# Kernel tuning notes

Measured on AMD Instinct MI355X. Metric: run time of the kernel, lower is better.

The kernel has to match this reference:

```python
import jax, jax.numpy as jnp
import numpy as np


def setup_inputs() -> dict:
    key = jax.random.key(0)
    k1, k2 = jax.random.split(key)
    B, T, D, K = 8, 4096, 256, 1024
    z = jax.random.normal(k1, (B, T, D), dtype=jnp.float32)
    codebook = jax.random.uniform(k2, (K, D), dtype=jnp.float32)
    return {"z": z, "codebook": codebook}


def reference(z, codebook):
    # Squared L2 distance via dot-product decomposition (same argmin as
    # the broadcasted squared-difference in the original module, without
    # materializing the (B,T,K,D) intermediate).
    #   ||z - c||^2 = ||z||^2 - 2 z.c + ||c||^2
    z_sq = jnp.sum(z * z, axis=-1, keepdims=True)            # (B,T,1)
    c_sq = jnp.sum(codebook * codebook, axis=-1)             # (K,)
    cross = jnp.einsum("btd,kd->btk", z, codebook)           # (B,T,K)
    l2_distance = z_sq - 2.0 * cross + c_sq                  # (B,T,K)
    codebook_indices = jnp.argmin(l2_distance, axis=-1)      # (B,T)
    z_q = codebook[codebook_indices]                         # (B,T,D)
    # Straight-through estimator
    z_q = z + jax.lax.stop_gradient(z_q - z)
    return (z_q, codebook_indices)
```

## Files before the change

### kernel.cpp

```cpp
#include <hip/hip_runtime.h>
#include <math.h>

#define NTOK   32768
#define NDIM   256
#define NCODE  1024
#define CHUNK  4096

typedef _Float16 f16x8 __attribute__((ext_vector_type(8)));
typedef float    f32x4 __attribute__((ext_vector_type(4)));

__device__ __forceinline__ void gld_lds16(const void* g, void* l) {
    __builtin_amdgcn_global_load_lds(
        (const __attribute__((address_space(1))) void*)g,
        (__attribute__((address_space(3))) void*)l, 16, 0, 0);
}

__global__ __launch_bounds__(256) void prep_cb(
        const float* __restrict__ cb,
        _Float16* __restrict__ ch, _Float16* __restrict__ cl,
        float* __restrict__ csq) {
    const int L   = blockIdx.x * 256 + threadIdx.x;
    const int row = L >> 5;
    const int g   = L & 31;

    const float* src = cb + (size_t)row * NDIM + g * 8;
    float4 a0 = *(const float4*)src;
    float4 a1 = *(const float4*)(src + 4);
    float v[8] = {a0.x, a0.y, a0.z, a0.w, a1.x, a1.y, a1.z, a1.w};
    f16x8 hi, lo;
    float s = 0.f;
    #pragma unroll
    for (int e = 0; e < 8; ++e) {
        _Float16 h = (_Float16)v[e];
        hi[e] = h;
        lo[e] = (_Float16)(v[e] - (float)h);
        s += v[e] * v[e];
    }
    const int r = row & 127;
    const size_t dst = (size_t)((row >> 7) * 8 + (g >> 2)) * CHUNK
                     + (r >> 4) * 512 + (g & 3) * 128 + (r & 15) * 8;
    *(f16x8*)&ch[dst] = hi;
    *(f16x8*)&cl[dst] = lo;
    #pragma unroll
    for (int off = 16; off > 0; off >>= 1) s += __shfl_down(s, off, 32);
    if ((threadIdx.x & 31) == 0) csq[row] = s;
}


#define STAGE(h, buf)                                                          \
    do {                                                                       \
        const size_t _sb = (size_t)(h) * 16384 + (size_t)tid * 8;              \
        _Pragma("unroll")                                                      \
        for (int _i = 0; _i < 4; ++_i) {                                       \
            gld_lds16(ch + _sb + _i * 4096, &Bs[buf][0][w * 512 + _i * 4096]); \
            gld_lds16(cl + _sb + _i * 4096, &Bs[buf][1][w * 512 + _i * 4096]); \
        }                                                                      \
    } while (0)

#define COMPUTE(kh, buf)                                                       \
    do {                                                                       \
        _Pragma("unroll")                                                      \
        for (int _k4 = 0; _k4 < 4; ++_k4) {                                    \
            f16x8 fbh[4], fbl[4];                                              \
            _Pragma("unroll")                                                  \
            for (int _t = 0; _t < 4; ++_t) {                                   \
                const int _off = _k4 * 4096 + (nx * 4 + _t) * 512              \
                               + quad * 128 + lr * 8;                          \
                fbh[_t] = *(const f16x8*)&Bs[buf][0][_off];                    \
                fbl[_t] = *(const f16x8*)&Bs[buf][1][_off];                    \
            }                                                                  \
            __builtin_amdgcn_s_setprio(1);                                     \
            _Pragma("unroll")                                                  \
            for (int _mt = 0; _mt < 2; ++_mt)                                  \
                _Pragma("unroll")                                              \
                for (int _t = 0; _t < 4; ++_t) {                               \
                    acc[_mt][_t] = __builtin_amdgcn_mfma_f32_16x16x32_f16(     \
                        ah[_mt][(kh) * 4 + _k4], fbh[_t], acc[_mt][_t], 0, 0, 0); \
                    acc[_mt][_t] = __builtin_amdgcn_mfma_f32_16x16x32_f16(     \
                        al[_mt][(kh) * 4 + _k4], fbh[_t], acc[_mt][_t], 0, 0, 0); \
                    acc[_mt][_t] = __builtin_amdgcn_mfma_f32_16x16x32_f16(     \
                        ah[_mt][(kh) * 4 + _k4], fbl[_t], acc[_mt][_t], 0, 0, 0); \
                }                                                              \
            __builtin_amdgcn_s_setprio(0);                                     \
        }                                                                      \
    } while (0)

__global__ __launch_bounds__(512, 2) void vq_main(
        const float* __restrict__ z,
        const _Float16* __restrict__ ch, const _Float16* __restrict__ cl,
        const float* __restrict__ csq, const float* __restrict__ cb,
        float* __restrict__ zq, float* __restrict__ io) {
    __shared__ _Float16 Bs[2][2][16384];

    const int tid  = threadIdx.x;
    const int w    = tid >> 6;
    const int lane = tid & 63;
    const int quad = lane >> 4, lr = lane & 15;
    const int my   = w >> 1, nx = w & 1;
    const int m0   = blockIdx.x * 128;

    STAGE(0, 0);

    f16x8 ah[2][8], al[2][8];
    #pragma unroll
    for (int mt = 0; mt < 2; ++mt) {
        const float* zp = z + (size_t)(m0 + my * 32 + mt * 16 + lr) * NDIM
                        + quad * 8;
        #pragma unroll
        for (int c = 0; c < 8; ++c) {
            float4 a0 = *(const float4*)(zp + c * 32);
            float4 a1 = *(const float4*)(zp + c * 32 + 4);
            float v[8] = {a0.x, a0.y, a0.z, a0.w, a1.x, a1.y, a1.z, a1.w};
            #pragma unroll
            for (int e = 0; e < 8; ++e) {
                _Float16 h = (_Float16)v[e];
                ah[mt][c][e] = h;
                al[mt][c][e] = (_Float16)(v[e] - (float)h);
            }
        }
    }

    float bv[2][4];
    int   bi[2][4];
    #pragma unroll
    for (int mt = 0; mt < 2; ++mt)
        #pragma unroll
        for (int r = 0; r < 4; ++r) { bv[mt][r] = INFINITY; bi[mt][r] = 0x7fffffff; }

    f32x4 acc[2][4];
    #pragma unroll
    for (int mt = 0; mt < 2; ++mt)
        #pragma unroll
        for (int t = 0; t < 4; ++t) acc[mt][t] = (f32x4){0.f, 0.f, 0.f, 0.f};

    for (int strip = 0; strip < 8; ++strip) {
        float cs[4];
        #pragma unroll
        for (int t = 0; t < 4; ++t)
            cs[t] = csq[strip * 128 + (nx * 4 + t) * 16 + lr];

        STAGE(2 * strip + 1, 1);
        asm volatile("s_waitcnt vmcnt(12)" ::: "memory");
        __builtin_amdgcn_s_barrier();
        __builtin_amdgcn_sched_barrier(0);
        COMPUTE(0, 0);
        __builtin_amdgcn_sched_barrier(0);
        __builtin_amdgcn_s_barrier();

        if (strip < 7) {
            STAGE(2 * strip + 2, 0);
            asm volatile("s_waitcnt vmcnt(8)" ::: "memory");
        } else {
            asm volatile("s_waitcnt vmcnt(0)" ::: "memory");
        }
        __builtin_amdgcn_s_barrier();
        __builtin_amdgcn_sched_barrier(0);
        COMPUTE(1, 1);
        __builtin_amdgcn_sched_barrier(0);
        __builtin_amdgcn_s_barrier();

        #pragma unroll
        for (int mt = 0; mt < 2; ++mt)
            #pragma unroll
            for (int r = 0; r < 4; ++r)
                #pragma unroll
                for (int t = 0; t < 4; ++t) {
                    float v = cs[t] - 2.0f * acc[mt][t][r];
                    int   n = strip * 128 + (nx * 4 + t) * 16 + lr;
                    if (v < bv[mt][r] || (v == bv[mt][r] && n < bi[mt][r])) {
                        bv[mt][r] = v; bi[mt][r] = n;
                    }
                }
        #pragma unroll
        for (int mt = 0; mt < 2; ++mt)
            #pragma unroll
            for (int t = 0; t < 4; ++t) acc[mt][t] = (f32x4){0.f, 0.f, 0.f, 0.f};
    }

    #pragma unroll
    for (int msk = 1; msk < 16; msk <<= 1)
        #pragma unroll
        for (int mt = 0; mt < 2; ++mt)
            #pragma unroll
            for (int r = 0; r < 4; ++r) {
                float ov = __shfl_xor(bv[mt][r], msk, 64);
                int   oi = __shfl_xor(bi[mt][r], msk, 64);
                if (ov < bv[mt][r] || (ov == bv[mt][r] && oi < bi[mt][r])) {
                    bv[mt][r] = ov; bi[mt][r] = oi;
                }
            }

    __syncthreads();
    float* sval  = (float*)&Bs[0][0][0];
    int*   sidx  = (int*)(sval + 256);
    int*   bestS = (int*)(sval + 512);

    if (lr == 0) {
        #pragma unroll
        for (int mt = 0; mt < 2; ++mt)
            #pragma unroll
            for (int r = 0; r < 4; ++r) {
                int row = my * 32 + mt * 16 + quad * 4 + r;
                sval[row * 2 + nx] = bv[mt][r];
                sidx[row * 2 + nx] = bi[mt][r];
            }
    }
    __syncthreads();

    if (tid < 128) {
        float v0 = sval[tid * 2], v1 = sval[tid * 2 + 1];
        int   i0 = sidx[tid * 2], i1 = sidx[tid * 2 + 1];
        bool take1 = (v1 < v0) || (v1 == v0 && i1 < i0);
        int best = take1 ? i1 : i0;
        bestS[tid] = best;
        io[m0 + tid] = (float)best;
    }
    __syncthreads();

    const int tr = tid >> 4, tc = tid & 15;
    #pragma unroll
    for (int p = 0; p < 4; ++p) {
        int row = p * 32 + tr;
        const float* src = cb + (size_t)bestS[row] * NDIM;
        float*       dst = zq + (size_t)(m0 + row) * NDIM;
        #pragma unroll
        for (int q = 0; q < 4; ++q) {
            int col = q * 64 + tc * 4;
            *(float4*)&dst[col] = *(const float4*)&src[col];
        }
    }
}

extern "C" void kernel_launch(void* const* d_in, const int* in_sizes, int n_in,
                              void* d_out, int out_size, void* d_ws, size_t ws_size,
                              hipStream_t stream) {
    const float* z  = (const float*)d_in[0];
    const float* cb = (const float*)d_in[1];

    float* zq = (float*)d_out;
    float* io = (float*)d_out + (size_t)NTOK * NDIM;

    _Float16* ch  = (_Float16*)d_ws;
    _Float16* cl  = ch + (size_t)NCODE * NDIM;
    float*    csq = (float*)(cl + (size_t)NCODE * NDIM);

    prep_cb<<<NCODE * 32 / 256, 256, 0, stream>>>(cb, ch, cl, csq);

    vq_main<<<NTOK / 128, 512, 0, stream>>>(z, ch, cl, csq, cb, zq, io);
}
```

Measured before the change: 151.6 us.

## Halve the token tile to 64 rows and split the codebook staging into quarter-strip stages

Each block now handles 64 tokens with 256 threads instead of 128 tokens with 512 threads. Codebook staging moves to quarter-strip (64-dim) double-buffered stages, which halves shared memory per block and gives four barrier-separated compute phases per strip. The sched_barrier fences are removed. The aim is more blocks per CU and a smaller LDS footprint to improve latency hiding, at the cost of twice as many blocks each re-reading the whole codebook, plus more barriers.

```diff
diff --git a/kernel.cpp b/kernel.cpp
--- a/kernel.cpp
+++ b/kernel.cpp
@@ -47,24 +47,26 @@
 }
 
 
-#define STAGE(h, buf)                                                          \
+#define STAGE(Q, buf)                                                          \
     do {                                                                       \
-        const size_t _sb = (size_t)(h) * 16384 + (size_t)tid * 8;              \
+        const size_t _sb = (size_t)(Q) * 8192 + w * 2048 + lane * 8;           \
+        const int    _lb = w * 2048;                                           \
         _Pragma("unroll")                                                      \
         for (int _i = 0; _i < 4; ++_i) {                                       \
-            gld_lds16(ch + _sb + _i * 4096, &Bs[buf][0][w * 512 + _i * 4096]); \
-            gld_lds16(cl + _sb + _i * 4096, &Bs[buf][1][w * 512 + _i * 4096]); \
+            gld_lds16(ch + _sb + _i * 512, &Bs[buf][0][_lb + _i * 512]);       \
+            gld_lds16(cl + _sb + _i * 512, &Bs[buf][1][_lb + _i * 512]);       \
         }                                                                      \
     } while (0)
 
-#define COMPUTE(kh, buf)                                                       \
+#define COMPUTE(q, buf)                                                        \
     do {                                                                       \
         _Pragma("unroll")                                                      \
-        for (int _k4 = 0; _k4 < 4; ++_k4) {                                    \
+        for (int _kc = 0; _kc < 2; ++_kc) {                                    \
+            const int _kg = (q) * 2 + _kc;                                     \
             f16x8 fbh[4], fbl[4];                                              \
             _Pragma("unroll")                                                  \
             for (int _t = 0; _t < 4; ++_t) {                                   \
-                const int _off = _k4 * 4096 + (nx * 4 + _t) * 512              \
+                const int _off = _kc * 4096 + (nx * 4 + _t) * 512              \
                                + quad * 128 + lr * 8;                          \
                 fbh[_t] = *(const f16x8*)&Bs[buf][0][_off];                    \
                 fbl[_t] = *(const f16x8*)&Bs[buf][1][_off];                    \
@@ -75,29 +77,29 @@
                 _Pragma("unroll")                                              \
                 for (int _t = 0; _t < 4; ++_t) {                               \
                     acc[_mt][_t] = __builtin_amdgcn_mfma_f32_16x16x32_f16(     \
-                        ah[_mt][(kh) * 4 + _k4], fbh[_t], acc[_mt][_t], 0, 0, 0); \
+                        ah[_mt][_kg], fbh[_t], acc[_mt][_t], 0, 0, 0);         \
                     acc[_mt][_t] = __builtin_amdgcn_mfma_f32_16x16x32_f16(     \
-                        al[_mt][(kh) * 4 + _k4], fbh[_t], acc[_mt][_t], 0, 0, 0); \
+                        al[_mt][_kg], fbh[_t], acc[_mt][_t], 0, 0, 0);         \
                     acc[_mt][_t] = __builtin_amdgcn_mfma_f32_16x16x32_f16(     \
-                        ah[_mt][(kh) * 4 + _k4], fbl[_t], acc[_mt][_t], 0, 0, 0); \
+                        ah[_mt][_kg], fbl[_t], acc[_mt][_t], 0, 0, 0);         \
                 }                                                              \
             __builtin_amdgcn_s_setprio(0);                                     \
         }                                                                      \
     } while (0)
 
-__global__ __launch_bounds__(512, 2) void vq_main(
+__global__ __launch_bounds__(256, 2) void vq_main(
         const float* __restrict__ z,
         const _Float16* __restrict__ ch, const _Float16* __restrict__ cl,
         const float* __restrict__ csq, const float* __restrict__ cb,
         float* __restrict__ zq, float* __restrict__ io) {
-    __shared__ _Float16 Bs[2][2][16384];
+    __shared__ _Float16 Bs[2][2][8192];
 
     const int tid  = threadIdx.x;
     const int w    = tid >> 6;
     const int lane = tid & 63;
     const int quad = lane >> 4, lr = lane & 15;
     const int my   = w >> 1, nx = w & 1;
-    const int m0   = blockIdx.x * 128;
+    const int m0   = blockIdx.x * 64;
 
     STAGE(0, 0);
 
@@ -134,29 +136,39 @@
         for (int t = 0; t < 4; ++t) acc[mt][t] = (f32x4){0.f, 0.f, 0.f, 0.f};
 
     for (int strip = 0; strip < 8; ++strip) {
+        const int Q0 = strip * 4;
+
         float cs[4];
         #pragma unroll
         for (int t = 0; t < 4; ++t)
             cs[t] = csq[strip * 128 + (nx * 4 + t) * 16 + lr];
 
-        STAGE(2 * strip + 1, 1);
+        STAGE(Q0 + 1, 1);
         asm volatile("s_waitcnt vmcnt(12)" ::: "memory");
         __builtin_amdgcn_s_barrier();
-        __builtin_amdgcn_sched_barrier(0);
         COMPUTE(0, 0);
-        __builtin_amdgcn_sched_barrier(0);
+        __builtin_amdgcn_s_barrier();
+
+        STAGE(Q0 + 2, 0);
+        asm volatile("s_waitcnt vmcnt(8)" ::: "memory");
+        __builtin_amdgcn_s_barrier();
+        COMPUTE(1, 1);
+        __builtin_amdgcn_s_barrier();
+
+        STAGE(Q0 + 3, 1);
+        asm volatile("s_waitcnt vmcnt(8)" ::: "memory");
+        __builtin_amdgcn_s_barrier();
+        COMPUTE(2, 0);
         __builtin_amdgcn_s_barrier();
 
         if (strip < 7) {
-            STAGE(2 * strip + 2, 0);
+            STAGE(Q0 + 4, 0);
             asm volatile("s_waitcnt vmcnt(8)" ::: "memory");
         } else {
             asm volatile("s_waitcnt vmcnt(0)" ::: "memory");
         }
         __builtin_amdgcn_s_barrier();
-        __builtin_amdgcn_sched_barrier(0);
-        COMPUTE(1, 1);
-        __builtin_amdgcn_sched_barrier(0);
+        COMPUTE(3, 1);
         __builtin_amdgcn_s_barrier();
 
         #pragma unroll
@@ -192,8 +204,8 @@
 
     __syncthreads();
     float* sval  = (float*)&Bs[0][0][0];
-    int*   sidx  = (int*)(sval + 256);
-    int*   bestS = (int*)(sval + 512);
+    int*   sidx  = (int*)&Bs[0][0][512];
+    int*   bestS = (int*)&Bs[0][0][1024];
 
     if (lr == 0) {
         #pragma unroll
@@ -207,7 +219,7 @@
     }
     __syncthreads();
 
-    if (tid < 128) {
+    if (tid < 64) {
         float v0 = sval[tid * 2], v1 = sval[tid * 2 + 1];
         int   i0 = sidx[tid * 2], i1 = sidx[tid * 2 + 1];
         bool take1 = (v1 < v0) || (v1 == v0 && i1 < i0);
@@ -220,7 +232,7 @@
     const int tr = tid >> 4, tc = tid & 15;
     #pragma unroll
     for (int p = 0; p < 4; ++p) {
-        int row = p * 32 + tr;
+        int row = p * 16 + tr;
         const float* src = cb + (size_t)bestS[row] * NDIM;
         float*       dst = zq + (size_t)(m0 + row) * NDIM;
         #pragma unroll
@@ -246,5 +258,5 @@
 
     prep_cb<<<NCODE * 32 / 256, 256, 0, stream>>>(cb, ch, cl, csq);
 
-    vq_main<<<NTOK / 128, 512, 0, stream>>>(z, ch, cl, csq, cb, zq, io);
-}
+    vq_main<<<NTOK / 64, 256, 0, stream>>>(z, ch, cl, csq, cb, zq, io);
+}
```

Result: faster. 138.3 us (-8.8%).
